# Kernel tuning notes

Measured on AMD Instinct MI355X. Metric: run time of the kernel, lower is better.

Reference implementation:

```python
import jax, jax.numpy as jnp
import numpy as np

C = 256  # in_dims
CQ = C // 2


def setup_inputs() -> dict:
    key = jax.random.key(0)
    ks = jax.random.split(key, 8)
    B, H, W = 8, 64, 64
    x = jax.random.normal(ks[0], (B, C, H, W), dtype=jnp.float32)
    s = 0.02
    Wq = jax.random.normal(ks[1], (CQ, C), dtype=jnp.float32) * s
    bq = jax.random.normal(ks[2], (CQ,), dtype=jnp.float32) * s
    Wk = jax.random.normal(ks[3], (CQ, C), dtype=jnp.float32) * s
    bk = jax.random.normal(ks[4], (CQ,), dtype=jnp.float32) * s
    Wv = jax.random.normal(ks[5], (C, C), dtype=jnp.float32) * s
    bv = jax.random.normal(ks[6], (C,), dtype=jnp.float32) * s
    gamma = jax.random.normal(ks[7], (1,), dtype=jnp.float32) * 0.5  # torch inits to 0; use nonzero for a meaningful test
    return {"x": x, "Wq": Wq, "bq": bq, "Wk": Wk, "bk": bk, "Wv": Wv, "bv": bv, "gamma": gamma}


def reference(x, Wq, bq, Wk, bk, Wv, bv, gamma):
    B, Ch, H, W = x.shape
    N = H * W
    xf = x.reshape(B, Ch, N)  # 1x1 conv == per-pixel linear over channels
    q = jnp.einsum('oc,bcn->bon', Wq, xf) + bq[None, :, None]  # [B, C/2, N]
    k = jnp.einsum('oc,bcn->bon', Wk, xf) + bk[None, :, None]  # [B, C/2, N]
    v = jnp.einsum('oc,bcn->bon', Wv, xf) + bv[None, :, None]  # [B, C,   N]
    # attention[b, m, n] = q_m . k_n ; softmax over dim=1 (the m axis), matching nn.Softmax(dim=1)
    scores = jnp.einsum('bcm,bcn->bmn', q, k)  # [B, N, N]
    attn = jax.nn.softmax(scores, axis=1)
    # torch.bmm(V, A^T)[b,c,m] = sum_n V[b,c,n] * A[b,m,n]
    out = jnp.einsum('bcn,bmn->bcm', v, attn)  # [B, C, N]
    return gamma * out.reshape(B, Ch, H, W) + x
```

## Files before the change

kernel.cpp:

```cpp
#include <hip/hip_runtime.h>


typedef unsigned short u16;
typedef __attribute__((ext_vector_type(8))) short bf16x8;
typedef __attribute__((ext_vector_type(4))) short bf16x4;
typedef __attribute__((ext_vector_type(4))) float f32x4;

__device__ __forceinline__ float bf2f(u16 u) {
  union { unsigned int i; float f; } v; v.i = ((unsigned int)u) << 16; return v.f;
}
__device__ __forceinline__ u16 f2bf(float f) {
  union { float f; unsigned int i; } v; v.f = f;
  unsigned int r = v.i + 0x7fffu + ((v.i >> 16) & 1u);
  return (u16)(r >> 16);
}

#define NB 8
#define NC 256
#define NCQ 128
#define NN 4096
#define LOG2E 1.4426950408889634f

__device__ __forceinline__ int scan_bad(const u16* p, int ns, int tid) {
  int bad = 0;
  for (int i = tid; i < ns; i += 256) {
    const int e = (p[2 * i] >> 7) & 0xff;
    bad |= (e >= 0x90) ? 1 : 0;
  }
  return bad;
}

__device__ __forceinline__ bf16x8 load8(const u16* pb, const float* pf,
                                        size_t off, bool f) {
  if (!f) return *(const bf16x8*)(pb + off);
  const float4 a = *(const float4*)(pf + off);
  const float4 b = *(const float4*)(pf + off + 4);
  bf16x8 r;
  r[0] = (short)f2bf(a.x); r[1] = (short)f2bf(a.y);
  r[2] = (short)f2bf(a.z); r[3] = (short)f2bf(a.w);
  r[4] = (short)f2bf(b.x); r[5] = (short)f2bf(b.y);
  r[6] = (short)f2bf(b.z); r[7] = (short)f2bf(b.w);
  return r;
}

__global__ __launch_bounds__(256, 2) void qkv_kernel(
    const void* xv, const void* Wqv, const void* bqv, const void* Wkv,
    const void* bkv, const void* Wvv, const void* bvv,
    u16* __restrict__ q2T, u16* __restrict__ kT, u16* __restrict__ vout) {
  __shared__ __align__(16) u16 xT[64][264];
  __shared__ int fl[8];
  const int tid = threadIdx.x;
  const int bid = blockIdx.x;
  const int b = bid & 7, n0 = (bid >> 3) << 6;

  if (tid < 8) fl[tid] = 0;
  __syncthreads();
  if (scan_bad((const u16*)xv, 256, tid)) fl[0] = 1;
  if (scan_bad((const u16*)Wqv, 64, tid)) fl[1] = 1;
  if (scan_bad((const u16*)Wkv, 64, tid)) fl[2] = 1;
  if (scan_bad((const u16*)Wvv, 64, tid)) fl[3] = 1;
  if (scan_bad((const u16*)bqv, 64, tid)) fl[4] = 1;
  if (scan_bad((const u16*)bkv, 64, tid)) fl[5] = 1;
  if (scan_bad((const u16*)bvv, 64, tid)) fl[6] = 1;
  __syncthreads();
  const bool fx = fl[0] != 0;

  {
    const int c = tid;
    const size_t roff = (size_t)(b * NC + c) * NN + n0;
    if (fx) {
      const float* xp = (const float*)xv + roff;
#pragma unroll
      for (int j = 0; j < 16; ++j) {
        const float4 t = *(const float4*)(xp + j * 4);
        xT[j * 4 + 0][c] = f2bf(t.x); xT[j * 4 + 1][c] = f2bf(t.y);
        xT[j * 4 + 2][c] = f2bf(t.z); xT[j * 4 + 3][c] = f2bf(t.w);
      }
    } else {
      const u16* xp = (const u16*)xv + roff;
#pragma unroll
      for (int j = 0; j < 8; ++j) {
        bf16x8 t = *(const bf16x8*)(xp + j * 8);
#pragma unroll
        for (int e = 0; e < 8; ++e) xT[j * 8 + e][c] = (u16)t[e];
      }
    }
  }
  __syncthreads();

  const int w = tid >> 6, lane = tid & 63, l15 = lane & 15, quad = lane >> 4;
  const u16* Wb; const float* Wf; const u16* Bb; const float* Bf;
  bool fW, fB; int obase = 0; u16* dstT = nullptr; float sc = 1.f;
  if (w == 0) {
    Wb = (const u16*)Wqv; Wf = (const float*)Wqv;
    Bb = (const u16*)bqv; Bf = (const float*)bqv;
    fW = fl[1]; fB = fl[4]; dstT = q2T; sc = LOG2E;
  } else if (w == 1) {
    Wb = (const u16*)Wkv; Wf = (const float*)Wkv;
    Bb = (const u16*)bkv; Bf = (const float*)bkv;
    fW = fl[2]; fB = fl[5]; dstT = kT;
  } else if (w == 2) {
    Wb = (const u16*)Wvv; Wf = (const float*)Wvv;
    Bb = (const u16*)bvv; Bf = (const float*)bvv;
    fW = fl[3]; fB = fl[6];
  } else {
    Wb = (const u16*)Wvv + 32768; Wf = (const float*)Wvv + 32768;
    Bb = (const u16*)bvv + 128;   Bf = (const float*)bvv + 128;
    fW = fl[3]; fB = fl[6]; obase = 128;
  }

  bf16x8 xfr[4][8];
#pragma unroll
  for (int nt = 0; nt < 4; ++nt) {
    const u16* xp = &xT[nt * 16 + l15][quad * 8];
#pragma unroll
    for (int ks = 0; ks < 8; ++ks) xfr[nt][ks] = *(const bf16x8*)(xp + ks * 32);
  }

  for (int ot = 0; ot < 8; ++ot) {
    bf16x8 wfr[8];
    const size_t wrow = (size_t)(ot * 16 + l15) * 256 + quad * 8;
#pragma unroll
    for (int ks = 0; ks < 8; ++ks) wfr[ks] = load8(Wb, Wf, wrow + ks * 32, fW);
    float bias[4];
    {
      const int boff = ot * 16 + quad * 4;
#pragma unroll
      for (int r = 0; r < 4; ++r)
        bias[r] = fB ? Bf[boff + r] : bf2f(Bb[boff + r]);
    }
#pragma unroll
    for (int nt = 0; nt < 4; ++nt) {
      f32x4 acc = {0.f, 0.f, 0.f, 0.f};
#pragma unroll
      for (int ks = 0; ks < 8; ++ks)
        acc = __builtin_amdgcn_mfma_f32_16x16x32_bf16(wfr[ks], xfr[nt][ks], acc, 0, 0, 0);
      const int n = n0 + nt * 16 + l15;
      if (w < 2) {
        ushort4 st;
        st.x = f2bf((acc[0] + bias[0]) * sc); st.y = f2bf((acc[1] + bias[1]) * sc);
        st.z = f2bf((acc[2] + bias[2]) * sc); st.w = f2bf((acc[3] + bias[3]) * sc);
        *(ushort4*)(dstT + ((size_t)(b * NN + n)) * NCQ + ot * 16 + quad * 4) = st;
      } else {
        const int c = obase + ot * 16 + quad * 4;
#pragma unroll
        for (int r = 0; r < 4; ++r)
          vout[((size_t)(b * NC + c + r)) * NN + n] = f2bf(acc[r] + bias[r]);
      }
    }
  }
}

__global__ __launch_bounds__(256, 2) void stats_kernel(
    const u16* __restrict__ q2T, const u16* __restrict__ kT,
    float* __restrict__ rbuf) {
  __shared__ float zbuf[4][64];
  const int bid = blockIdx.x;
  const int b = bid & 7, n0 = (bid >> 3) << 6;
  const int tid = threadIdx.x;
  const int w = tid >> 6, lane = tid & 63, l15 = lane & 15, quad = lane >> 4;

  bf16x8 kf[4][4];
  {
    const u16* kp = kT + ((size_t)(b * NN + n0 + l15)) * NCQ + quad * 8;
#pragma unroll
    for (int nt = 0; nt < 4; ++nt)
#pragma unroll
      for (int ks = 0; ks < 4; ++ks) {
        kf[nt][ks] = *(const bf16x8*)(kp + (size_t)(nt * 16) * NCQ + ks * 32);
        asm volatile("" : "+v"(kf[nt][ks]));
      }
  }

  float Z[4] = {0.f, 0.f, 0.f, 0.f};
  for (int it = 0; it < 64; ++it) {
    const int mb = w * 1024 + it * 16;
    const u16* qp = q2T + ((size_t)(b * NN + mb + l15)) * NCQ + quad * 8;
    bf16x8 af[4];
#pragma unroll
    for (int ks = 0; ks < 4; ++ks) af[ks] = *(const bf16x8*)(qp + ks * 32);
#pragma unroll
    for (int nt = 0; nt < 4; ++nt) {
      f32x4 acc = {0.f, 0.f, 0.f, 0.f};
#pragma unroll
      for (int ks = 0; ks < 4; ++ks)
        acc = __builtin_amdgcn_mfma_f32_16x16x32_bf16(af[ks], kf[nt][ks], acc, 0, 0, 0);
      Z[nt] += __builtin_amdgcn_exp2f(acc[0]) + __builtin_amdgcn_exp2f(acc[1]) +
               __builtin_amdgcn_exp2f(acc[2]) + __builtin_amdgcn_exp2f(acc[3]);
    }
  }
#pragma unroll
  for (int nt = 0; nt < 4; ++nt) {
    float z = Z[nt];
    z += __shfl_xor(z, 16, 64);
    z += __shfl_xor(z, 32, 64);
    Z[nt] = z;
  }
  if (lane < 16) {
#pragma unroll
    for (int nt = 0; nt < 4; ++nt) zbuf[w][nt * 16 + lane] = Z[nt];
  }
  __syncthreads();
  if (tid < 64) {
    const float z = zbuf[0][tid] + zbuf[1][tid] + zbuf[2][tid] + zbuf[3][tid];
    rbuf[b * NN + n0 + tid] = 1.0f / z;
  }
}

__global__ __launch_bounds__(256, 4) void scale_kernel(
    u16* __restrict__ vr, const float* __restrict__ rbuf) {
  const int flat = (blockIdx.x * 256 + threadIdx.x) * 8;
  const int n = flat & (NN - 1);
  const int b = flat >> 20;
  const float4 r0 = *(const float4*)(rbuf + (b << 12) + n);
  const float4 r1 = *(const float4*)(rbuf + (b << 12) + n + 4);
  const ushort4 a0 = *(const ushort4*)(vr + flat);
  const ushort4 a1 = *(const ushort4*)(vr + flat + 4);
  ushort4 s0, s1;
  s0.x = f2bf(bf2f(a0.x) * r0.x); s0.y = f2bf(bf2f(a0.y) * r0.y);
  s0.z = f2bf(bf2f(a0.z) * r0.z); s0.w = f2bf(bf2f(a0.w) * r0.w);
  s1.x = f2bf(bf2f(a1.x) * r1.x); s1.y = f2bf(bf2f(a1.y) * r1.y);
  s1.z = f2bf(bf2f(a1.z) * r1.z); s1.w = f2bf(bf2f(a1.w) * r1.w);
  *(ushort4*)(vr + flat) = s0;
  *(ushort4*)(vr + flat + 4) = s1;
}

__global__ __launch_bounds__(256, 4) void out_kernel(
    const u16* __restrict__ q2T, const u16* __restrict__ kT,
    const u16* __restrict__ vr,
    const void* xv, const void* gv,
    const void* bqv, const void* bkv, const void* bvv,
    void* outv) {
  __shared__ __align__(16) u16 et[2][4][16][68];
  __shared__ int fl[2];
  const int tid = threadIdx.x;
  if (tid < 2) fl[tid] = 0;
  __syncthreads();
  if (scan_bad((const u16*)xv, 256, tid)) fl[0] = 1;
  if (scan_bad((const u16*)bqv, 64, tid) | scan_bad((const u16*)bkv, 64, tid) |
      scan_bad((const u16*)bvv, 64, tid)) fl[1] = 1;

  const int bid = blockIdx.x;
  const int b = bid & 7;
  const int r7 = bid >> 3;
  const int ch = r7 & 1;
  const int m0 = (r7 >> 1) << 6;
  const int w = tid >> 6, lane = tid & 63, l15 = lane & 15, quad = lane >> 4;

  bf16x8 qf[4][4];
  {
    const u16* qp = q2T + ((size_t)(b * NN + m0 + l15)) * NCQ + quad * 8;
#pragma unroll
    for (int mg = 0; mg < 4; ++mg)
#pragma unroll
      for (int ks = 0; ks < 4; ++ks) {
        qf[mg][ks] = *(const bf16x8*)(qp + (size_t)(mg * 16) * NCQ + ks * 32);
        asm volatile("" : "+v"(qf[mg][ks]));
      }
  }
  __syncthreads();
  const bool fx = fl[0] != 0, fg = fl[1] != 0;

  f32x4 acc[8];
#pragma unroll
  for (int i = 0; i < 8; ++i) acc[i] = (f32x4){0.f, 0.f, 0.f, 0.f};

  const u16* kb = kT + ((size_t)(b * NN + w * 16 + l15)) * NCQ + quad * 8;
  const u16* vb = vr + ((size_t)(b * NC + ch * 128 + w * 32 + l15)) * NN + quad * 8;

  for (int n0 = 0; n0 < NN; n0 += 64) {
    const int pp = (n0 >> 6) & 1;
    bf16x8 kf[4], vf[4];
#pragma unroll
    for (int ks = 0; ks < 4; ++ks)
      kf[ks] = *(const bf16x8*)(kb + (size_t)n0 * NCQ + ks * 32);
#pragma unroll
    for (int ct = 0; ct < 2; ++ct)
#pragma unroll
      for (int ns = 0; ns < 2; ++ns)
        vf[ct * 2 + ns] =
            *(const bf16x8*)(vb + (size_t)(ct * 16) * NN + n0 + ns * 32);
#pragma unroll
    for (int mg = 0; mg < 4; ++mg) {
      f32x4 s = {0.f, 0.f, 0.f, 0.f};
#pragma unroll
      for (int ks = 0; ks < 4; ++ks)
        s = __builtin_amdgcn_mfma_f32_16x16x32_bf16(kf[ks], qf[mg][ks], s, 0, 0, 0);
      bf16x4 ev;
      ev[0] = (short)f2bf(__builtin_amdgcn_exp2f(s[0]));
      ev[1] = (short)f2bf(__builtin_amdgcn_exp2f(s[1]));
      ev[2] = (short)f2bf(__builtin_amdgcn_exp2f(s[2]));
      ev[3] = (short)f2bf(__builtin_amdgcn_exp2f(s[3]));
      *(bf16x4*)(&et[pp][mg][l15][w * 16 + quad * 4]) = ev;
    }
    __syncthreads();
#pragma unroll
    for (int mg = 0; mg < 4; ++mg)
#pragma unroll
      for (int ns = 0; ns < 2; ++ns) {
        const bf16x8 af = *(const bf16x8*)(&et[pp][mg][l15][ns * 32 + quad * 8]);
#pragma unroll
        for (int ct = 0; ct < 2; ++ct)
          acc[mg * 2 + ct] = __builtin_amdgcn_mfma_f32_16x16x32_bf16(
              af, vf[ct * 2 + ns], acc[mg * 2 + ct], 0, 0, 0);
      }
  }

  const float g = fg ? ((const float*)gv)[0] : bf2f(((const u16*)gv)[0]);
#pragma unroll
  for (int mg = 0; mg < 4; ++mg)
#pragma unroll
    for (int ct = 0; ct < 2; ++ct) {
      const int c = ch * 128 + w * 32 + ct * 16 + l15;
      const int m = m0 + mg * 16 + quad * 4;
      const size_t base = ((size_t)(b * NC + c)) * NN + m;
      const f32x4 a = acc[mg * 2 + ct];
      if (fx) {
        const float4 xl = *(const float4*)((const float*)xv + base);
        float4 st;
        st.x = g * a[0] + xl.x; st.y = g * a[1] + xl.y;
        st.z = g * a[2] + xl.z; st.w = g * a[3] + xl.w;
        *(float4*)((float*)outv + base) = st;
      } else {
        const ushort4 xl = *(const ushort4*)((const u16*)xv + base);
        ushort4 st;
        st.x = f2bf(g * a[0] + bf2f(xl.x));
        st.y = f2bf(g * a[1] + bf2f(xl.y));
        st.z = f2bf(g * a[2] + bf2f(xl.z));
        st.w = f2bf(g * a[3] + bf2f(xl.w));
        *(ushort4*)((u16*)outv + base) = st;
      }
    }
}

extern "C" void kernel_launch(void* const* d_in, const int* in_sizes, int n_in,
                              void* d_out, int out_size, void* d_ws, size_t ws_size,
                              hipStream_t stream) {
  const size_t NEED = 33554432u;
  if (ws_size < NEED) return;

  char* ws = (char*)d_ws;
  u16* q2 = (u16*)(ws);
  u16* kk = (u16*)(ws + 8388608);
  u16* vv = (u16*)(ws + 16777216);
  float* rbuf = (ws_size >= NEED + 131072u) ? (float*)(ws + NEED) : (float*)d_out;

  qkv_kernel<<<512, 256, 0, stream>>>(d_in[0], d_in[1], d_in[2], d_in[3],
                                      d_in[4], d_in[5], d_in[6], q2, kk, vv);
  stats_kernel<<<512, 256, 0, stream>>>(q2, kk, rbuf);
  scale_kernel<<<4096, 256, 0, stream>>>(vv, rbuf);
  out_kernel<<<1024, 256, 0, stream>>>(q2, kk, vv, d_in[0], d_in[7],
                                       d_in[2], d_in[4], d_in[6], d_out);
}
```

Measured before the change: 441.1 us.

## Widen attention blocks to 512 threads covering all channels and 128 query rows

The output kernel now has each 512-thread block handle 128 query rows and all 256 channels. The exp(QK) tile is computed once and shared across every channel instead of being recomputed for each channel half, which halves the score MFMA and exp work. The stats kernel gives each wave its own 16 keys and streams all queries, which removes the shared-memory reduction. The trade-off is 256 blocks at one block per CU, so occupancy drops and each thread holds 16 accumulator tiles, raising register pressure.

Result: slower. 526.0 us (+19.3%).

```diff
diff --git a/kernel.cpp b/kernel.cpp
--- a/kernel.cpp
+++ b/kernel.cpp
@@ -151,60 +151,46 @@
   }
 }
 
-__global__ __launch_bounds__(256, 2) void stats_kernel(
+__global__ __launch_bounds__(512, 1) void stats_kernel(
     const u16* __restrict__ q2T, const u16* __restrict__ kT,
     float* __restrict__ rbuf) {
-  __shared__ float zbuf[4][64];
   const int bid = blockIdx.x;
-  const int b = bid & 7, n0 = (bid >> 3) << 6;
+  const int b = bid & 7, n0 = (bid >> 3) << 7;
   const int tid = threadIdx.x;
   const int w = tid >> 6, lane = tid & 63, l15 = lane & 15, quad = lane >> 4;
 
-  bf16x8 kf[4][4];
+  bf16x8 kf[4];
   {
-    const u16* kp = kT + ((size_t)(b * NN + n0 + l15)) * NCQ + quad * 8;
-#pragma unroll
-    for (int nt = 0; nt < 4; ++nt)
-#pragma unroll
-      for (int ks = 0; ks < 4; ++ks) {
-        kf[nt][ks] = *(const bf16x8*)(kp + (size_t)(nt * 16) * NCQ + ks * 32);
-        asm volatile("" : "+v"(kf[nt][ks]));
-      }
-  }
-
-  float Z[4] = {0.f, 0.f, 0.f, 0.f};
-  for (int it = 0; it < 64; ++it) {
-    const int mb = w * 1024 + it * 16;
+    const u16* kp = kT + ((size_t)(b * NN + n0 + w * 16 + l15)) * NCQ + quad * 8;
+#pragma unroll
+    for (int ks = 0; ks < 4; ++ks) {
+      kf[ks] = *(const bf16x8*)(kp + ks * 32);
+      asm volatile("" : "+v"(kf[ks]));
+    }
+  }
+
+  float Z = 0.f;
+  for (int mb = 0; mb < NN; mb += 64) {
     const u16* qp = q2T + ((size_t)(b * NN + mb + l15)) * NCQ + quad * 8;
-    bf16x8 af[4];
-#pragma unroll
-    for (int ks = 0; ks < 4; ++ks) af[ks] = *(const bf16x8*)(qp + ks * 32);
-#pragma unroll
-    for (int nt = 0; nt < 4; ++nt) {
-      f32x4 acc = {0.f, 0.f, 0.f, 0.f};
+    bf16x8 af[4][4];
+#pragma unroll
+    for (int u = 0; u < 4; ++u)
 #pragma unroll
       for (int ks = 0; ks < 4; ++ks)
-        acc = __builtin_amdgcn_mfma_f32_16x16x32_bf16(af[ks], kf[nt][ks], acc, 0, 0, 0);
-      Z[nt] += __builtin_amdgcn_exp2f(acc[0]) + __builtin_amdgcn_exp2f(acc[1]) +
-               __builtin_amdgcn_exp2f(acc[2]) + __builtin_amdgcn_exp2f(acc[3]);
-    }
-  }
-#pragma unroll
-  for (int nt = 0; nt < 4; ++nt) {
-    float z = Z[nt];
-    z += __shfl_xor(z, 16, 64);
-    z += __shfl_xor(z, 32, 64);
-    Z[nt] = z;
-  }
-  if (lane < 16) {
-#pragma unroll
-    for (int nt = 0; nt < 4; ++nt) zbuf[w][nt * 16 + lane] = Z[nt];
-  }
-  __syncthreads();
-  if (tid < 64) {
-    const float z = zbuf[0][tid] + zbuf[1][tid] + zbuf[2][tid] + zbuf[3][tid];
-    rbuf[b * NN + n0 + tid] = 1.0f / z;
-  }
+        af[u][ks] = *(const bf16x8*)(qp + (size_t)(u * 16) * NCQ + ks * 32);
+#pragma unroll
+    for (int u = 0; u < 4; ++u) {
+      f32x4 s = {0.f, 0.f, 0.f, 0.f};
+#pragma unroll
+      for (int ks = 0; ks < 4; ++ks)
+        s = __builtin_amdgcn_mfma_f32_16x16x32_bf16(af[u][ks], kf[ks], s, 0, 0, 0);
+      Z += __builtin_amdgcn_exp2f(s[0]) + __builtin_amdgcn_exp2f(s[1]) +
+           __builtin_amdgcn_exp2f(s[2]) + __builtin_amdgcn_exp2f(s[3]);
+    }
+  }
+  Z += __shfl_xor(Z, 16, 64);
+  Z += __shfl_xor(Z, 32, 64);
+  if (lane < 16) rbuf[b * NN + n0 + w * 16 + l15] = 1.0f / Z;
 }
 
 __global__ __launch_bounds__(256, 4) void scale_kernel(
@@ -225,13 +211,13 @@
   *(ushort4*)(vr + flat + 4) = s1;
 }
 
-__global__ __launch_bounds__(256, 4) void out_kernel(
+__global__ __launch_bounds__(512, 1) void out_kernel(
     const u16* __restrict__ q2T, const u16* __restrict__ kT,
     const u16* __restrict__ vr,
     const void* xv, const void* gv,
     const void* bqv, const void* bkv, const void* bvv,
     void* outv) {
-  __shared__ __align__(16) u16 et[2][4][16][68];
+  __shared__ __align__(16) u16 et[2][8][16][68];
   __shared__ int fl[2];
   const int tid = threadIdx.x;
   if (tid < 2) fl[tid] = 0;
@@ -242,14 +228,13 @@
 
   const int bid = blockIdx.x;
   const int b = bid & 7;
-  const int r7 = bid >> 3;
-  const int ch = r7 & 1;
-  const int m0 = (r7 >> 1) << 6;
+  const int m0 = (bid >> 3) << 7;
   const int w = tid >> 6, lane = tid & 63, l15 = lane & 15, quad = lane >> 4;
+  const int mh = w >> 2, nq = w & 3;
 
   bf16x8 qf[4][4];
   {
-    const u16* qp = q2T + ((size_t)(b * NN + m0 + l15)) * NCQ + quad * 8;
+    const u16* qp = q2T + ((size_t)(b * NN + m0 + mh * 64 + l15)) * NCQ + quad * 8;
 #pragma unroll
     for (int mg = 0; mg < 4; ++mg)
 #pragma unroll
@@ -261,12 +246,12 @@
   __syncthreads();
   const bool fx = fl[0] != 0, fg = fl[1] != 0;
 
-  f32x4 acc[8];
-#pragma unroll
-  for (int i = 0; i < 8; ++i) acc[i] = (f32x4){0.f, 0.f, 0.f, 0.f};
-
-  const u16* kb = kT + ((size_t)(b * NN + w * 16 + l15)) * NCQ + quad * 8;
-  const u16* vb = vr + ((size_t)(b * NC + ch * 128 + w * 32 + l15)) * NN + quad * 8;
+  f32x4 acc[16];
+#pragma unroll
+  for (int i = 0; i < 16; ++i) acc[i] = (f32x4){0.f, 0.f, 0.f, 0.f};
+
+  const u16* kb = kT + ((size_t)(b * NN + nq * 16 + l15)) * NCQ + quad * 8;
+  const u16* vb = vr + ((size_t)(b * NC + w * 32 + l15)) * NN + quad * 8;
 
   for (int n0 = 0; n0 < NN; n0 += 64) {
     const int pp = (n0 >> 6) & 1;
@@ -291,11 +276,11 @@
       ev[1] = (short)f2bf(__builtin_amdgcn_exp2f(s[1]));
       ev[2] = (short)f2bf(__builtin_amdgcn_exp2f(s[2]));
       ev[3] = (short)f2bf(__builtin_amdgcn_exp2f(s[3]));
-      *(bf16x4*)(&et[pp][mg][l15][w * 16 + quad * 4]) = ev;
+      *(bf16x4*)(&et[pp][mh * 4 + mg][l15][nq * 16 + quad * 4]) = ev;
     }
     __syncthreads();
 #pragma unroll
-    for (int mg = 0; mg < 4; ++mg)
+    for (int mg = 0; mg < 8; ++mg)
 #pragma unroll
       for (int ns = 0; ns < 2; ++ns) {
         const bf16x8 af = *(const bf16x8*)(&et[pp][mg][l15][ns * 32 + quad * 8]);
@@ -308,10 +293,10 @@
 
   const float g = fg ? ((const float*)gv)[0] : bf2f(((const u16*)gv)[0]);
 #pragma unroll
-  for (int mg = 0; mg < 4; ++mg)
+  for (int mg = 0; mg < 8; ++mg)
 #pragma unroll
     for (int ct = 0; ct < 2; ++ct) {
-      const int c = ch * 128 + w * 32 + ct * 16 + l15;
+      const int c = w * 32 + ct * 16 + l15;
       const int m = m0 + mg * 16 + quad * 4;
       const size_t base = ((size_t)(b * NC + c)) * NN + m;
       const f32x4 a = acc[mg * 2 + ct];
@@ -347,8 +332,8 @@
 
   qkv_kernel<<<512, 256, 0, stream>>>(d_in[0], d_in[1], d_in[2], d_in[3],
                                       d_in[4], d_in[5], d_in[6], q2, kk, vv);
-  stats_kernel<<<512, 256, 0, stream>>>(q2, kk, rbuf);
+  stats_kernel<<<256, 512, 0, stream>>>(q2, kk, rbuf);
   scale_kernel<<<4096, 256, 0, stream>>>(vv, rbuf);
-  out_kernel<<<1024, 256, 0, stream>>>(q2, kk, vv, d_in[0], d_in[7],
-                                       d_in[2], d_in[4], d_in[6], d_out);
-}
+  out_kernel<<<256, 512, 0, stream>>>(q2, kk, vv, d_in[0], d_in[7],
+                                      d_in[2], d_in[4], d_in[6], d_out);
+}
```

## Software-prefetch K/Q fragments and stage Q tile in LDS

Applied to the files above, without the earlier changes.

The column-sum kernel is unrolled by two with double-buffered Q fragment registers, so the next Q tile's global load is issued before the current MFMAs run. In the output kernel the Q tile moves from registers into padded shared memory, freeing VGPRs. K fragments are double-buffered one 64-column step ahead, with the loop unrolled by two over the et ping-pong buffers. This hides global load latency behind MFMA and exp work, at the cost of extra LDS reads of Q every iteration and some added register pressure from the prefetch buffers.

After: 438.4 us. No clear change (-0.6%).

```diff
diff --git a/kernel.cpp b/kernel.cpp
--- a/kernel.cpp
+++ b/kernel.cpp
@@ -172,19 +172,39 @@
       }
   }
 
+  const u16* qbase = q2T + ((size_t)(b * NN + w * 1024 + l15)) * NCQ + quad * 8;
   float Z[4] = {0.f, 0.f, 0.f, 0.f};
-  for (int it = 0; it < 64; ++it) {
-    const int mb = w * 1024 + it * 16;
-    const u16* qp = q2T + ((size_t)(b * NN + mb + l15)) * NCQ + quad * 8;
-    bf16x8 af[4];
-#pragma unroll
-    for (int ks = 0; ks < 4; ++ks) af[ks] = *(const bf16x8*)(qp + ks * 32);
+  bf16x8 afA[4], afB[4];
+#pragma unroll
+  for (int ks = 0; ks < 4; ++ks) afA[ks] = *(const bf16x8*)(qbase + ks * 32);
+
+  for (int it = 0; it < 64; it += 2) {
+    {
+      const u16* qp = qbase + (size_t)((it + 1) * 16) * NCQ;
+#pragma unroll
+      for (int ks = 0; ks < 4; ++ks) afB[ks] = *(const bf16x8*)(qp + ks * 32);
+    }
 #pragma unroll
     for (int nt = 0; nt < 4; ++nt) {
       f32x4 acc = {0.f, 0.f, 0.f, 0.f};
 #pragma unroll
       for (int ks = 0; ks < 4; ++ks)
-        acc = __builtin_amdgcn_mfma_f32_16x16x32_bf16(af[ks], kf[nt][ks], acc, 0, 0, 0);
+        acc = __builtin_amdgcn_mfma_f32_16x16x32_bf16(afA[ks], kf[nt][ks], acc, 0, 0, 0);
+      Z[nt] += __builtin_amdgcn_exp2f(acc[0]) + __builtin_amdgcn_exp2f(acc[1]) +
+               __builtin_amdgcn_exp2f(acc[2]) + __builtin_amdgcn_exp2f(acc[3]);
+    }
+    {
+      const int it2 = (it + 2) & 63;
+      const u16* qp = qbase + (size_t)(it2 * 16) * NCQ;
+#pragma unroll
+      for (int ks = 0; ks < 4; ++ks) afA[ks] = *(const bf16x8*)(qp + ks * 32);
+    }
+#pragma unroll
+    for (int nt = 0; nt < 4; ++nt) {
+      f32x4 acc = {0.f, 0.f, 0.f, 0.f};
+#pragma unroll
+      for (int ks = 0; ks < 4; ++ks)
+        acc = __builtin_amdgcn_mfma_f32_16x16x32_bf16(afB[ks], kf[nt][ks], acc, 0, 0, 0);
       Z[nt] += __builtin_amdgcn_exp2f(acc[0]) + __builtin_amdgcn_exp2f(acc[1]) +
                __builtin_amdgcn_exp2f(acc[2]) + __builtin_amdgcn_exp2f(acc[3]);
     }
@@ -231,6 +251,7 @@
     const void* xv, const void* gv,
     const void* bqv, const void* bkv, const void* bvv,
     void* outv) {
+  __shared__ __align__(16) u16 qs[64][136];
   __shared__ __align__(16) u16 et[2][4][16][68];
   __shared__ int fl[2];
   const int tid = threadIdx.x;
@@ -247,16 +268,12 @@
   const int m0 = (r7 >> 1) << 6;
   const int w = tid >> 6, lane = tid & 63, l15 = lane & 15, quad = lane >> 4;
 
-  bf16x8 qf[4][4];
   {
-    const u16* qp = q2T + ((size_t)(b * NN + m0 + l15)) * NCQ + quad * 8;
-#pragma unroll
-    for (int mg = 0; mg < 4; ++mg)
-#pragma unroll
-      for (int ks = 0; ks < 4; ++ks) {
-        qf[mg][ks] = *(const bf16x8*)(qp + (size_t)(mg * 16) * NCQ + ks * 32);
-        asm volatile("" : "+v"(qf[mg][ks]));
-      }
+    const int mm = tid >> 2, ck = (tid & 3) * 32;
+    const u16* src = q2T + ((size_t)(b * NN + m0 + mm)) * NCQ + ck;
+#pragma unroll
+    for (int j = 0; j < 4; ++j)
+      *(bf16x8*)(&qs[mm][ck + j * 8]) = *(const bf16x8*)(src + j * 8);
   }
   __syncthreads();
   const bool fx = fl[0] != 0, fg = fl[1] != 0;
@@ -268,42 +285,94 @@
   const u16* kb = kT + ((size_t)(b * NN + w * 16 + l15)) * NCQ + quad * 8;
   const u16* vb = vr + ((size_t)(b * NC + ch * 128 + w * 32 + l15)) * NN + quad * 8;
 
-  for (int n0 = 0; n0 < NN; n0 += 64) {
-    const int pp = (n0 >> 6) & 1;
-    bf16x8 kf[4], vf[4];
-#pragma unroll
-    for (int ks = 0; ks < 4; ++ks)
-      kf[ks] = *(const bf16x8*)(kb + (size_t)n0 * NCQ + ks * 32);
-#pragma unroll
-    for (int ct = 0; ct < 2; ++ct)
-#pragma unroll
-      for (int ns = 0; ns < 2; ++ns)
-        vf[ct * 2 + ns] =
-            *(const bf16x8*)(vb + (size_t)(ct * 16) * NN + n0 + ns * 32);
-#pragma unroll
-    for (int mg = 0; mg < 4; ++mg) {
-      f32x4 s = {0.f, 0.f, 0.f, 0.f};
+  bf16x8 kfA[4], kfB[4];
+#pragma unroll
+  for (int ks = 0; ks < 4; ++ks)
+    kfA[ks] = *(const bf16x8*)(kb + ks * 32);
+
+  for (int n0 = 0; n0 < NN; n0 += 128) {
+    {
+      bf16x8 vf[4];
+#pragma unroll
+      for (int ct = 0; ct < 2; ++ct)
+#pragma unroll
+        for (int ns = 0; ns < 2; ++ns)
+          vf[ct * 2 + ns] =
+              *(const bf16x8*)(vb + (size_t)(ct * 16) * NN + n0 + ns * 32);
 #pragma unroll
       for (int ks = 0; ks < 4; ++ks)
-        s = __builtin_amdgcn_mfma_f32_16x16x32_bf16(kf[ks], qf[mg][ks], s, 0, 0, 0);
-      bf16x4 ev;
-      ev[0] = (short)f2bf(__builtin_amdgcn_exp2f(s[0]));
-      ev[1] = (short)f2bf(__builtin_amdgcn_exp2f(s[1]));
-      ev[2] = (short)f2bf(__builtin_amdgcn_exp2f(s[2]));
-      ev[3] = (short)f2bf(__builtin_amdgcn_exp2f(s[3]));
-      *(bf16x4*)(&et[pp][mg][l15][w * 16 + quad * 4]) = ev;
-    }
-    __syncthreads();
-#pragma unroll
-    for (int mg = 0; mg < 4; ++mg)
-#pragma unroll
-      for (int ns = 0; ns < 2; ++ns) {
-        const bf16x8 af = *(const bf16x8*)(&et[pp][mg][l15][ns * 32 + quad * 8]);
-#pragma unroll
-        for (int ct = 0; ct < 2; ++ct)
-          acc[mg * 2 + ct] = __builtin_amdgcn_mfma_f32_16x16x32_bf16(
-              af, vf[ct * 2 + ns], acc[mg * 2 + ct], 0, 0, 0);
-      }
+        kfB[ks] = *(const bf16x8*)(kb + (size_t)(n0 + 64) * NCQ + ks * 32);
+#pragma unroll
+      for (int mg = 0; mg < 4; ++mg) {
+        f32x4 s = {0.f, 0.f, 0.f, 0.f};
+#pragma unroll
+        for (int ks = 0; ks < 4; ++ks) {
+          const bf16x8 qfr =
+              *(const bf16x8*)(&qs[mg * 16 + l15][quad * 8 + ks * 32]);
+          s = __builtin_amdgcn_mfma_f32_16x16x32_bf16(kfA[ks], qfr, s, 0, 0, 0);
+        }
+        bf16x4 ev;
+        ev[0] = (short)f2bf(__builtin_amdgcn_exp2f(s[0]));
+        ev[1] = (short)f2bf(__builtin_amdgcn_exp2f(s[1]));
+        ev[2] = (short)f2bf(__builtin_amdgcn_exp2f(s[2]));
+        ev[3] = (short)f2bf(__builtin_amdgcn_exp2f(s[3]));
+        *(bf16x4*)(&et[0][mg][l15][w * 16 + quad * 4]) = ev;
+      }
+      __syncthreads();
+#pragma unroll
+      for (int mg = 0; mg < 4; ++mg)
+#pragma unroll
+        for (int ns = 0; ns < 2; ++ns) {
+          const bf16x8 af = *(const bf16x8*)(&et[0][mg][l15][ns * 32 + quad * 8]);
+#pragma unroll
+          for (int ct = 0; ct < 2; ++ct)
+            acc[mg * 2 + ct] = __builtin_amdgcn_mfma_f32_16x16x32_bf16(
+                af, vf[ct * 2 + ns], acc[mg * 2 + ct], 0, 0, 0);
+        }
+    }
+    {
+      const int n1 = n0 + 64;
+      bf16x8 vf[4];
+#pragma unroll
+      for (int ct = 0; ct < 2; ++ct)
+#pragma unroll
+        for (int ns = 0; ns < 2; ++ns)
+          vf[ct * 2 + ns] =
+              *(const bf16x8*)(vb + (size_t)(ct * 16) * NN + n1 + ns * 32);
+      {
+        const int n2 = (n0 + 128) & (NN - 1);
+#pragma unroll
+        for (int ks = 0; ks < 4; ++ks)
+          kfA[ks] = *(const bf16x8*)(kb + (size_t)n2 * NCQ + ks * 32);
+      }
+#pragma unroll
+      for (int mg = 0; mg < 4; ++mg) {
+        f32x4 s = {0.f, 0.f, 0.f, 0.f};
+#pragma unroll
+        for (int ks = 0; ks < 4; ++ks) {
+          const bf16x8 qfr =
+              *(const bf16x8*)(&qs[mg * 16 + l15][quad * 8 + ks * 32]);
+          s = __builtin_amdgcn_mfma_f32_16x16x32_bf16(kfB[ks], qfr, s, 0, 0, 0);
+        }
+        bf16x4 ev;
+        ev[0] = (short)f2bf(__builtin_amdgcn_exp2f(s[0]));
+        ev[1] = (short)f2bf(__builtin_amdgcn_exp2f(s[1]));
+        ev[2] = (short)f2bf(__builtin_amdgcn_exp2f(s[2]));
+        ev[3] = (short)f2bf(__builtin_amdgcn_exp2f(s[3]));
+        *(bf16x4*)(&et[1][mg][l15][w * 16 + quad * 4]) = ev;
+      }
+      __syncthreads();
+#pragma unroll
+      for (int mg = 0; mg < 4; ++mg)
+#pragma unroll
+        for (int ns = 0; ns < 2; ++ns) {
+          const bf16x8 af = *(const bf16x8*)(&et[1][mg][l15][ns * 32 + quad * 8]);
+#pragma unroll
+          for (int ct = 0; ct < 2; ++ct)
+            acc[mg * 2 + ct] = __builtin_amdgcn_mfma_f32_16x16x32_bf16(
+                af, vf[ct * 2 + ns], acc[mg * 2 + ct], 0, 0, 0);
+        }
+    }
   }
 
   const float g = fg ? ((const float*)gv)[0] : bf2f(((const u16*)gv)[0]);
```

## Raise occupancy: 8-wave stats blocks and shared-memory Q tile in out kernel

Applied to the files above, without the earlier changes.

The stats kernel now runs 512 threads per block, with each of eight waves covering 512 query rows instead of four waves covering 1024, and the cross-wave reduction widens to match. The out kernel moves the Q tile out of registers into LDS, reloading fragments per MFMA. It drops the double-buffered exp tile for a single buffer plus a second barrier, and raises launch bounds to 6 blocks per CU. The aim is to free VGPRs for more resident waves to hide latency, at the cost of extra LDS reads and one more barrier per iteration.

Result: no change. 437.1 us (-0.9%).

```diff
diff --git a/kernel.cpp b/kernel.cpp
--- a/kernel.cpp
+++ b/kernel.cpp
@@ -151,10 +151,10 @@
   }
 }
 
-__global__ __launch_bounds__(256, 2) void stats_kernel(
+__global__ __launch_bounds__(512, 4) void stats_kernel(
     const u16* __restrict__ q2T, const u16* __restrict__ kT,
     float* __restrict__ rbuf) {
-  __shared__ float zbuf[4][64];
+  __shared__ float zbuf[8][64];
   const int bid = blockIdx.x;
   const int b = bid & 7, n0 = (bid >> 3) << 6;
   const int tid = threadIdx.x;
@@ -172,10 +172,10 @@
       }
   }
 
+  const u16* qbase = q2T + ((size_t)(b * NN + w * 512 + l15)) * NCQ + quad * 8;
   float Z[4] = {0.f, 0.f, 0.f, 0.f};
-  for (int it = 0; it < 64; ++it) {
-    const int mb = w * 1024 + it * 16;
-    const u16* qp = q2T + ((size_t)(b * NN + mb + l15)) * NCQ + quad * 8;
+  for (int it = 0; it < 32; ++it) {
+    const u16* qp = qbase + (size_t)(it * 16) * NCQ;
     bf16x8 af[4];
 #pragma unroll
     for (int ks = 0; ks < 4; ++ks) af[ks] = *(const bf16x8*)(qp + ks * 32);
@@ -202,7 +202,9 @@
   }
   __syncthreads();
   if (tid < 64) {
-    const float z = zbuf[0][tid] + zbuf[1][tid] + zbuf[2][tid] + zbuf[3][tid];
+    float z = 0.f;
+#pragma unroll
+    for (int ww = 0; ww < 8; ++ww) z += zbuf[ww][tid];
     rbuf[b * NN + n0 + tid] = 1.0f / z;
   }
 }
@@ -225,13 +227,14 @@
   *(ushort4*)(vr + flat + 4) = s1;
 }
 
-__global__ __launch_bounds__(256, 4) void out_kernel(
+__global__ __launch_bounds__(256, 6) void out_kernel(
     const u16* __restrict__ q2T, const u16* __restrict__ kT,
     const u16* __restrict__ vr,
     const void* xv, const void* gv,
     const void* bqv, const void* bkv, const void* bvv,
     void* outv) {
-  __shared__ __align__(16) u16 et[2][4][16][68];
+  __shared__ __align__(16) u16 qs[64][136];
+  __shared__ __align__(16) u16 et[4][16][68];
   __shared__ int fl[2];
   const int tid = threadIdx.x;
   if (tid < 2) fl[tid] = 0;
@@ -247,16 +250,12 @@
   const int m0 = (r7 >> 1) << 6;
   const int w = tid >> 6, lane = tid & 63, l15 = lane & 15, quad = lane >> 4;
 
-  bf16x8 qf[4][4];
   {
-    const u16* qp = q2T + ((size_t)(b * NN + m0 + l15)) * NCQ + quad * 8;
-#pragma unroll
-    for (int mg = 0; mg < 4; ++mg)
-#pragma unroll
-      for (int ks = 0; ks < 4; ++ks) {
-        qf[mg][ks] = *(const bf16x8*)(qp + (size_t)(mg * 16) * NCQ + ks * 32);
-        asm volatile("" : "+v"(qf[mg][ks]));
-      }
+    const int mm = tid >> 2, ck = (tid & 3) * 32;
+    const u16* src = q2T + ((size_t)(b * NN + m0 + mm)) * NCQ + ck;
+#pragma unroll
+    for (int j = 0; j < 4; ++j)
+      *(bf16x8*)(&qs[mm][ck + j * 8]) = *(const bf16x8*)(src + j * 8);
   }
   __syncthreads();
   const bool fx = fl[0] != 0, fg = fl[1] != 0;
@@ -269,7 +268,6 @@
   const u16* vb = vr + ((size_t)(b * NC + ch * 128 + w * 32 + l15)) * NN + quad * 8;
 
   for (int n0 = 0; n0 < NN; n0 += 64) {
-    const int pp = (n0 >> 6) & 1;
     bf16x8 kf[4], vf[4];
 #pragma unroll
     for (int ks = 0; ks < 4; ++ks)
@@ -284,26 +282,30 @@
     for (int mg = 0; mg < 4; ++mg) {
       f32x4 s = {0.f, 0.f, 0.f, 0.f};
 #pragma unroll
-      for (int ks = 0; ks < 4; ++ks)
-        s = __builtin_amdgcn_mfma_f32_16x16x32_bf16(kf[ks], qf[mg][ks], s, 0, 0, 0);
+      for (int ks = 0; ks < 4; ++ks) {
+        const bf16x8 qfr =
+            *(const bf16x8*)(&qs[mg * 16 + l15][quad * 8 + ks * 32]);
+        s = __builtin_amdgcn_mfma_f32_16x16x32_bf16(kf[ks], qfr, s, 0, 0, 0);
+      }
       bf16x4 ev;
       ev[0] = (short)f2bf(__builtin_amdgcn_exp2f(s[0]));
       ev[1] = (short)f2bf(__builtin_amdgcn_exp2f(s[1]));
       ev[2] = (short)f2bf(__builtin_amdgcn_exp2f(s[2]));
       ev[3] = (short)f2bf(__builtin_amdgcn_exp2f(s[3]));
-      *(bf16x4*)(&et[pp][mg][l15][w * 16 + quad * 4]) = ev;
+      *(bf16x4*)(&et[mg][l15][w * 16 + quad * 4]) = ev;
     }
     __syncthreads();
 #pragma unroll
     for (int mg = 0; mg < 4; ++mg)
 #pragma unroll
       for (int ns = 0; ns < 2; ++ns) {
-        const bf16x8 af = *(const bf16x8*)(&et[pp][mg][l15][ns * 32 + quad * 8]);
+        const bf16x8 af = *(const bf16x8*)(&et[mg][l15][ns * 32 + quad * 8]);
 #pragma unroll
         for (int ct = 0; ct < 2; ++ct)
           acc[mg * 2 + ct] = __builtin_amdgcn_mfma_f32_16x16x32_bf16(
               af, vf[ct * 2 + ns], acc[mg * 2 + ct], 0, 0, 0);
       }
+    __syncthreads();
   }
 
   const float g = fg ? ((const float*)gv)[0] : bf2f(((const u16*)gv)[0]);
@@ -347,7 +349,7 @@
 
   qkv_kernel<<<512, 256, 0, stream>>>(d_in[0], d_in[1], d_in[2], d_in[3],
                                       d_in[4], d_in[5], d_in[6], q2, kk, vv);
-  stats_kernel<<<512, 256, 0, stream>>>(q2, kk, rbuf);
+  stats_kernel<<<512, 512, 0, stream>>>(q2, kk, rbuf);
   scale_kernel<<<4096, 256, 0, stream>>>(vv, rbuf);
   out_kernel<<<1024, 256, 0, stream>>>(q2, kk, vv, d_in[0], d_in[7],
                                        d_in[2], d_in[4], d_in[6], d_out);
```
